# Optimization experiments

Hardware: AMD Instinct MI355X
Metric: run time of the kernel (lower is better)

Reference implementation:

```python
import jax, jax.numpy as jnp
import numpy as np
import math

N_ITEMS = 200000
N_USERS = 100000
D = 128
E_II = 3200000
E_UI = 1600000


def spmm(src, dst, val, x, n_rows):
    # out[i] = sum_{e: dst[e]==i} val[e] * x[src[e]]
    return jax.ops.segment_sum(val[:, None] * x[src], dst, num_segments=n_rows)


def leaky_relu(x):
    return jnp.where(x >= 0, x, 0.2 * x)


def setup_inputs() -> dict:
    key = jax.random.key(0)
    ks = jax.random.split(key, 16)
    d = {}
    d["b"] = 2
    d["items_emb"] = jax.random.normal(ks[0], (N_ITEMS, D), dtype=jnp.float32) * 0.1
    for i, rel in enumerate(["p2p_in", "p2p_out", "e2p_in"]):
        d[f"src_{rel}"] = jax.random.randint(ks[1 + 3 * i], (E_II,), 0, N_ITEMS, dtype=jnp.int32)
        d[f"dst_{rel}"] = jax.random.randint(ks[2 + 3 * i], (E_II,), 0, N_ITEMS, dtype=jnp.int32)
        d[f"val_{rel}"] = jax.random.uniform(ks[3 + 3 * i], (E_II,), dtype=jnp.float32) / 16.0
    d["src_ui"] = jax.random.randint(ks[10], (E_UI,), 0, N_ITEMS, dtype=jnp.int32)
    d["dst_ui"] = jax.random.randint(ks[11], (E_UI,), 0, N_USERS, dtype=jnp.int32)
    d["val_ui"] = jax.random.uniform(ks[12], (E_UI,), dtype=jnp.float32) / 16.0
    s = 1.0 / math.sqrt(D)
    d["I_p2p_in"] = jax.random.normal(ks[13], (D, D), dtype=jnp.float32) * s
    d["I_p2p_out"] = jax.random.normal(ks[14], (D, D), dtype=jnp.float32) * s
    d["I_e2p_in"] = jax.random.normal(ks[15], (D, D), dtype=jnp.float32) * s
    return d


def reference(b, items_emb, src_p2p_in, dst_p2p_in, val_p2p_in,
              src_p2p_out, dst_p2p_out, val_p2p_out,
              src_e2p_in, dst_e2p_in, val_e2p_in,
              src_ui, dst_ui, val_ui,
              I_p2p_in, I_p2p_out, I_e2p_in):
    assert b == 2  # static branch, matches torch `if b == 2`
    x = items_emb
    n = x.shape[0]
    inv_sqrt_d = 1.0 / math.sqrt(x.shape[1])

    # multi-relation sparse aggregation (torch.spmm)
    nb_in = spmm(src_p2p_in, dst_p2p_in, val_p2p_in, x, n)
    nb_out = spmm(src_p2p_out, dst_p2p_out, val_p2p_out, x, n)
    nb_e2p = spmm(src_e2p_in, dst_e2p_in, val_e2p_in, x, n)

    # gated attention over relations
    h_in = leaky_relu((x * nb_in) @ I_p2p_in)
    h_out = leaky_relu((x * nb_out) @ I_p2p_out)
    h_e2p = leaky_relu((x * nb_e2p) @ I_e2p_in)
    s_in = jnp.sum(h_in, axis=1) * inv_sqrt_d
    s_out = jnp.sum(h_out, axis=1) * inv_sqrt_d
    s_e2p = jnp.sum(h_e2p, axis=1) * inv_sqrt_d
    score = jax.nn.softmax(jnp.stack((s_in, s_out, s_e2p), axis=1), axis=1)  # [n,3]
    neighbor = (nb_in * score[:, 0:1]
                + nb_out * score[:, 1:2]
                + nb_e2p * score[:, 2:3])

    # uiGNN: user embeddings from item embeddings
    u_emb = spmm(src_ui, dst_ui, val_ui, x, N_USERS)
    return (u_emb, neighbor)
```

## Files before the change

kernel.cpp:

```cpp
#include <hip/hip_runtime.h>

#define D 128
#define N_ITEMS 200000
#define N_USERS 100000
#define TI 64

#define INV_SQRT_D 0.088388347648318447f

__global__ __launch_bounds__(256) void hist_kernel(
    const int* __restrict__ dst, unsigned* __restrict__ counts, int E)
{
    int e = blockIdx.x * 256 + threadIdx.x;
    if (e < E) atomicAdd(&counts[dst[e]], 1u);
}

__global__ __launch_bounds__(256) void scan1_kernel(
    const unsigned* __restrict__ counts, unsigned* __restrict__ offsets,
    unsigned* __restrict__ blocksums, int n)
{
    __shared__ unsigned s[256];
    int tid = threadIdx.x;
    int i = blockIdx.x * 256 + tid;
    unsigned v = (i < n) ? counts[i] : 0u;
    s[tid] = v; __syncthreads();
    #pragma unroll
    for (int off = 1; off < 256; off <<= 1) {
        unsigned t = (tid >= off) ? s[tid - off] : 0u;
        __syncthreads();
        s[tid] += t;
        __syncthreads();
    }
    if (i < n) offsets[i] = s[tid] - v;
    if (tid == 255) blocksums[blockIdx.x] = s[255];
}

__global__ __launch_bounds__(1024) void scan2_kernel(
    unsigned* __restrict__ blocksums, int nb)
{
    __shared__ unsigned s[1024];
    int tid = threadIdx.x;
    unsigned v = (tid < nb) ? blocksums[tid] : 0u;
    s[tid] = v; __syncthreads();
    #pragma unroll
    for (int off = 1; off < 1024; off <<= 1) {
        unsigned t = (tid >= off) ? s[tid - off] : 0u;
        __syncthreads();
        s[tid] += t;
        __syncthreads();
    }
    if (tid < nb) blocksums[tid] = s[tid] - v;
}

__global__ __launch_bounds__(256) void scan3_kernel(
    unsigned* __restrict__ offsets, unsigned* __restrict__ cursor,
    const unsigned* __restrict__ blocksums, int n, unsigned Etot)
{
    int i = blockIdx.x * 256 + threadIdx.x;
    if (i < n) {
        unsigned o = offsets[i] + blocksums[blockIdx.x];
        offsets[i] = o;
        cursor[i] = o;
    }
    if (i == 0) offsets[n] = Etot;
}

__global__ __launch_bounds__(256) void scatter_kernel(
    const int* __restrict__ src, const int* __restrict__ dst,
    const float* __restrict__ val, unsigned* __restrict__ cursor,
    int2* __restrict__ pairs, int E)
{
    int e = blockIdx.x * 256 + threadIdx.x;
    if (e >= E) return;
    unsigned pos = atomicAdd(&cursor[dst[e]], 1u);
    pairs[pos] = make_int2(src[e], __float_as_int(val[e]));
}

__global__ __launch_bounds__(256) void gather_spmm_kernel(
    const unsigned* __restrict__ offsets, const int2* __restrict__ pairs,
    const float4* __restrict__ x4, float4* __restrict__ out4, int nrows)
{
    int row = blockIdx.x * 8 + (threadIdx.x >> 5);
    if (row >= nrows) return;
    int lane = threadIdx.x & 31;
    unsigned j = offsets[row], end = offsets[row + 1];
    float4 acc = make_float4(0.f, 0.f, 0.f, 0.f);
    for (; j + 2 <= end; j += 2) {
        int2 p0 = pairs[j];
        int2 p1 = pairs[j + 1];
        float4 a = x4[(size_t)p0.x * 32 + lane];
        float4 b = x4[(size_t)p1.x * 32 + lane];
        float v0 = __int_as_float(p0.y), v1 = __int_as_float(p1.y);
        acc.x = fmaf(v0, a.x, acc.x); acc.y = fmaf(v0, a.y, acc.y);
        acc.z = fmaf(v0, a.z, acc.z); acc.w = fmaf(v0, a.w, acc.w);
        acc.x = fmaf(v1, b.x, acc.x); acc.y = fmaf(v1, b.y, acc.y);
        acc.z = fmaf(v1, b.z, acc.z); acc.w = fmaf(v1, b.w, acc.w);
    }
    if (j < end) {
        int2 p0 = pairs[j];
        float4 a = x4[(size_t)p0.x * 32 + lane];
        float v0 = __int_as_float(p0.y);
        acc.x = fmaf(v0, a.x, acc.x); acc.y = fmaf(v0, a.y, acc.y);
        acc.z = fmaf(v0, a.z, acc.z); acc.w = fmaf(v0, a.w, acc.w);
    }
    out4[(size_t)row * 32 + lane] = acc;
}

__global__ __launch_bounds__(256, 4) void score_combine_kernel(
    const float4* __restrict__ x4,
    float4* __restrict__ nb0,
    const float4* __restrict__ nb1, const float4* __restrict__ nb2,
    const float* __restrict__ I0, const float* __restrict__ I1,
    const float* __restrict__ I2)
{
    __shared__ float Tt[D * 65];
    __shared__ float Sred[3 * 4 * 64];
    __shared__ float Wl[TI * 3];

    const int tid  = threadIdx.x;
    const int lane = tid & 63;
    const int wv   = __builtin_amdgcn_readfirstlane(tid >> 6);
    const int ilo  = tid >> 5;
    const int dd4  = tid & 31;
    const int itemBase = blockIdx.x * TI;

    float4 xr[8];
    #pragma unroll
    for (int it = 0; it < 8; ++it) {
        int il = it * 8 + ilo;
        xr[it] = x4[(size_t)(itemBase + il) * 32 + dd4];
    }

    const float4* nbs[3] = {(const float4*)nb0, nb1, nb2};
    const float*  Is[3]  = {I0, I1, I2};

    for (int rel = 0; rel < 3; ++rel) {
        __syncthreads();
        const float4* nbp = nbs[rel];
        #pragma unroll
        for (int it = 0; it < 8; ++it) {
            int il = it * 8 + ilo;
            float4 b = nbp[(size_t)(itemBase + il) * 32 + dd4];
            float4 a = xr[it];
            int base = (dd4 * 4) * 65 + il;
            Tt[base]       = a.x * b.x;
            Tt[base + 65]  = a.y * b.y;
            Tt[base + 130] = a.z * b.z;
            Tt[base + 195] = a.w * b.w;
        }
        __syncthreads();

        const float4* Iw4 = (const float4*)Is[rel] + wv * 8;
        float4 acc[8];
        #pragma unroll
        for (int c = 0; c < 8; ++c) acc[c] = make_float4(0.f, 0.f, 0.f, 0.f);

        #pragma unroll 2
        for (int k = 0; k < D; ++k) {
            float tv = Tt[k * 65 + lane];
            #pragma unroll
            for (int c = 0; c < 8; ++c) {
                float4 iv = Iw4[k * 32 + c];
                acc[c].x = fmaf(tv, iv.x, acc[c].x);
                acc[c].y = fmaf(tv, iv.y, acc[c].y);
                acc[c].z = fmaf(tv, iv.z, acc[c].z);
                acc[c].w = fmaf(tv, iv.w, acc[c].w);
            }
        }

        float s = 0.f;
        #pragma unroll
        for (int c = 0; c < 8; ++c) {
            s += fmaxf(acc[c].x, 0.2f * acc[c].x);
            s += fmaxf(acc[c].y, 0.2f * acc[c].y);
            s += fmaxf(acc[c].z, 0.2f * acc[c].z);
            s += fmaxf(acc[c].w, 0.2f * acc[c].w);
        }
        Sred[rel * 256 + wv * 64 + lane] = s;
    }
    __syncthreads();

    if (tid < TI) {
        float sr[3];
        #pragma unroll
        for (int r = 0; r < 3; ++r)
            sr[r] = (Sred[r * 256 + tid] + Sred[r * 256 + 64 + tid] +
                     Sred[r * 256 + 128 + tid] + Sred[r * 256 + 192 + tid])
                    * INV_SQRT_D;
        float m = fmaxf(sr[0], fmaxf(sr[1], sr[2]));
        float e0 = expf(sr[0] - m), e1 = expf(sr[1] - m), e2 = expf(sr[2] - m);
        float inv = 1.f / (e0 + e1 + e2);
        Wl[tid * 3 + 0] = e0 * inv;
        Wl[tid * 3 + 1] = e1 * inv;
        Wl[tid * 3 + 2] = e2 * inv;
    }
    __syncthreads();

    #pragma unroll
    for (int it = 0; it < 8; ++it) {
        int il = it * 8 + ilo;
        size_t g = (size_t)(itemBase + il) * 32 + dd4;
        float w0 = Wl[il * 3 + 0], w1 = Wl[il * 3 + 1], w2 = Wl[il * 3 + 2];
        float4 a = nb0[g], b = nb1[g], c = nb2[g];
        float4 r;
        r.x = fmaf(w0, a.x, fmaf(w1, b.x, w2 * c.x));
        r.y = fmaf(w0, a.y, fmaf(w1, b.y, w2 * c.y));
        r.z = fmaf(w0, a.z, fmaf(w1, b.z, w2 * c.z));
        r.w = fmaf(w0, a.w, fmaf(w1, b.w, w2 * c.w));
        nb0[g] = r;
    }
}

extern "C" void kernel_launch(void* const* d_in, const int* in_sizes, int n_in,
                              void* d_out, int out_size, void* d_ws, size_t ws_size,
                              hipStream_t stream) {
    const float* x       = (const float*)d_in[1];
    const int*   src0    = (const int*)d_in[2];
    const int*   dst0    = (const int*)d_in[3];
    const float* val0    = (const float*)d_in[4];
    const int*   src1    = (const int*)d_in[5];
    const int*   dst1    = (const int*)d_in[6];
    const float* val1    = (const float*)d_in[7];
    const int*   src2    = (const int*)d_in[8];
    const int*   dst2    = (const int*)d_in[9];
    const float* val2    = (const float*)d_in[10];
    const int*   src_ui  = (const int*)d_in[11];
    const int*   dst_ui  = (const int*)d_in[12];
    const float* val_ui  = (const float*)d_in[13];
    const float* I0      = (const float*)d_in[14];
    const float* I1      = (const float*)d_in[15];
    const float* I2      = (const float*)d_in[16];

    const int E_ii = in_sizes[2];
    const int E_ui = in_sizes[11];

    float* u_emb = (float*)d_out;
    float* nb0   = (float*)d_out + (size_t)N_USERS * D;

    float*    nb1       = (float*)d_ws;
    float*    nb2       = nb1 + (size_t)N_ITEMS * D;
    unsigned* cc        = (unsigned*)(nb2 + (size_t)N_ITEMS * D);
    unsigned* offsets   = cc + N_ITEMS;
    unsigned* blocksums = offsets + N_ITEMS + 1;
    uintptr_t pu        = ((uintptr_t)(blocksums + 1024) + 15) & ~(uintptr_t)15;
    int2*     pairs_ui  = (int2*)pu;
    int2*     pairs_ii  = (int2*)d_out;

    auto build_and_gather = [&](const int* src, const int* dst, const float* val,
                                int E, int nrows, int2* pairs, float* out) {
        hipMemsetAsync(cc, 0, (size_t)nrows * sizeof(unsigned), stream);
        int gE = (E + 255) / 256;
        int gN = (nrows + 255) / 256;
        hist_kernel<<<gE, 256, 0, stream>>>(dst, cc, E);
        scan1_kernel<<<gN, 256, 0, stream>>>(cc, offsets, blocksums, nrows);
        scan2_kernel<<<1, 1024, 0, stream>>>(blocksums, gN);
        scan3_kernel<<<gN, 256, 0, stream>>>(offsets, cc, blocksums, nrows, (unsigned)E);
        scatter_kernel<<<gE, 256, 0, stream>>>(src, dst, val, cc, pairs, E);
        gather_spmm_kernel<<<(nrows + 7) / 8, 256, 0, stream>>>(
            offsets, pairs, (const float4*)x, (float4*)out, nrows);
    };

    build_and_gather(src0, dst0, val0, E_ii, N_ITEMS, pairs_ii, nb0);
    build_and_gather(src1, dst1, val1, E_ii, N_ITEMS, pairs_ii, nb1);
    build_and_gather(src2, dst2, val2, E_ii, N_ITEMS, pairs_ii, nb2);

    score_combine_kernel<<<N_ITEMS / TI, 256, 0, stream>>>(
        (const float4*)x, (float4*)nb0, (const float4*)nb1, (const float4*)nb2,
        I0, I1, I2);

    build_and_gather(src_ui, dst_ui, val_ui, E_ui, N_USERS, pairs_ui, u_emb);
}
```

Before: 2.558 ms.

## Batch CSR histogram and scan across all relations, unroll gather, swizzle LDS

All four relations (three item-item and one user-item) now share one padded count array. A single histogram kernel, one memset and one three-kernel scan build CSR offsets for every relation, replacing four separate build pipelines. The histogram and scatter kernels handle two edges per thread, and the gather SpMM loop is unrolled to four edges with a higher occupancy hint. The score kernel's transposed LDS tile uses an XOR swizzle to reduce bank conflicts. In exchange, the code relies on padded per-relation offsets and reuses nb2 as the pairs buffer for the user relation, which is safe only because nb2 is consumed before that scatter runs.

```diff
diff --git a/kernel.cpp b/kernel.cpp
--- a/kernel.cpp
+++ b/kernel.cpp
@@ -5,23 +5,48 @@
 #define N_USERS 100000
 #define TI 64
 
+#define PADN 200192
+#define PADU 100096
+#define NT   (3 * PADN + PADU)
+#define NBLK (NT / 256)
+#define RSB0 0
+#define RSB1 (PADN / 256)
+#define RSB2 (2 * PADN / 256)
+#define RSB3 (3 * PADN / 256)
+
 #define INV_SQRT_D 0.088388347648318447f
 
-__global__ __launch_bounds__(256) void hist_kernel(
-    const int* __restrict__ dst, unsigned* __restrict__ counts, int E)
-{
-    int e = blockIdx.x * 256 + threadIdx.x;
-    if (e < E) atomicAdd(&counts[dst[e]], 1u);
+__global__ __launch_bounds__(256) void hist_all_kernel(
+    const int* __restrict__ d0, const int* __restrict__ d1,
+    const int* __restrict__ d2, const int* __restrict__ du,
+    unsigned* __restrict__ counts, int Eii, int Eui, int gh)
+{
+    int bi = blockIdx.x;
+    const int* dp; int E; int base; int b0;
+    if (bi < 3 * gh) {
+        int r = bi / gh;
+        dp = (r == 0) ? d0 : (r == 1 ? d1 : d2);
+        E = Eii; base = r * PADN; b0 = r * gh;
+    } else {
+        dp = du; E = Eui; base = 3 * PADN; b0 = 3 * gh;
+    }
+    int e = ((bi - b0) * 256 + threadIdx.x) * 2;
+    if (e + 2 <= E) {
+        int a = dp[e], b = dp[e + 1];
+        atomicAdd(&counts[base + a], 1u);
+        atomicAdd(&counts[base + b], 1u);
+    } else if (e < E) {
+        atomicAdd(&counts[base + dp[e]], 1u);
+    }
 }
 
 __global__ __launch_bounds__(256) void scan1_kernel(
-    const unsigned* __restrict__ counts, unsigned* __restrict__ offsets,
-    unsigned* __restrict__ blocksums, int n)
+    unsigned* __restrict__ data, unsigned* __restrict__ blocksums)
 {
     __shared__ unsigned s[256];
     int tid = threadIdx.x;
     int i = blockIdx.x * 256 + tid;
-    unsigned v = (i < n) ? counts[i] : 0u;
+    unsigned v = data[i];
     s[tid] = v; __syncthreads();
     #pragma unroll
     for (int off = 1; off < 256; off <<= 1) {
@@ -30,17 +55,23 @@
         s[tid] += t;
         __syncthreads();
     }
-    if (i < n) offsets[i] = s[tid] - v;
+    data[i] = s[tid] - v;
     if (tid == 255) blocksums[blockIdx.x] = s[255];
 }
 
 __global__ __launch_bounds__(1024) void scan2_kernel(
-    unsigned* __restrict__ blocksums, int nb)
+    unsigned* __restrict__ bs, int nb)
 {
     __shared__ unsigned s[1024];
     int tid = threadIdx.x;
-    unsigned v = (tid < nb) ? blocksums[tid] : 0u;
-    s[tid] = v; __syncthreads();
+    int base = tid * 4;
+    unsigned v[4]; unsigned tot = 0;
+    #pragma unroll
+    for (int t = 0; t < 4; ++t) {
+        v[t] = (base + t < nb) ? bs[base + t] : 0u;
+        tot += v[t];
+    }
+    s[tid] = tot; __syncthreads();
     #pragma unroll
     for (int off = 1; off < 1024; off <<= 1) {
         unsigned t = (tid >= off) ? s[tid - off] : 0u;
@@ -48,20 +79,25 @@
         s[tid] += t;
         __syncthreads();
     }
-    if (tid < nb) blocksums[tid] = s[tid] - v;
+    unsigned run = s[tid] - tot;
+    #pragma unroll
+    for (int t = 0; t < 4; ++t) {
+        unsigned old = v[t];
+        if (base + t < nb) bs[base + t] = run;
+        run += old;
+    }
 }
 
 __global__ __launch_bounds__(256) void scan3_kernel(
-    unsigned* __restrict__ offsets, unsigned* __restrict__ cursor,
-    const unsigned* __restrict__ blocksums, int n, unsigned Etot)
+    unsigned* __restrict__ offs, unsigned* __restrict__ cursor,
+    const unsigned* __restrict__ bs)
 {
     int i = blockIdx.x * 256 + threadIdx.x;
-    if (i < n) {
-        unsigned o = offsets[i] + blocksums[blockIdx.x];
-        offsets[i] = o;
-        cursor[i] = o;
-    }
-    if (i == 0) offsets[n] = Etot;
+    int rel = (i < 3 * PADN) ? (i / PADN) : 3;
+    int rsb = (rel == 0) ? RSB0 : (rel == 1 ? RSB1 : (rel == 2 ? RSB2 : RSB3));
+    unsigned o = offs[i] + bs[blockIdx.x] - bs[rsb];
+    offs[i] = o;
+    cursor[i] = o;
 }
 
 __global__ __launch_bounds__(256) void scatter_kernel(
@@ -69,13 +105,22 @@
     const float* __restrict__ val, unsigned* __restrict__ cursor,
     int2* __restrict__ pairs, int E)
 {
-    int e = blockIdx.x * 256 + threadIdx.x;
-    if (e >= E) return;
-    unsigned pos = atomicAdd(&cursor[dst[e]], 1u);
-    pairs[pos] = make_int2(src[e], __float_as_int(val[e]));
-}
-
-__global__ __launch_bounds__(256) void gather_spmm_kernel(
+    int e = (blockIdx.x * 256 + threadIdx.x) * 2;
+    if (e + 2 <= E) {
+        int s0 = src[e], s1 = src[e + 1];
+        int d0 = dst[e], d1 = dst[e + 1];
+        float v0 = val[e], v1 = val[e + 1];
+        unsigned p0 = atomicAdd(&cursor[d0], 1u);
+        unsigned p1 = atomicAdd(&cursor[d1], 1u);
+        pairs[p0] = make_int2(s0, __float_as_int(v0));
+        pairs[p1] = make_int2(s1, __float_as_int(v1));
+    } else if (e < E) {
+        unsigned p = atomicAdd(&cursor[dst[e]], 1u);
+        pairs[p] = make_int2(src[e], __float_as_int(val[e]));
+    }
+}
+
+__global__ __launch_bounds__(256, 8) void gather_spmm_kernel(
     const unsigned* __restrict__ offsets, const int2* __restrict__ pairs,
     const float4* __restrict__ x4, float4* __restrict__ out4, int nrows)
 {
@@ -84,7 +129,27 @@
     int lane = threadIdx.x & 31;
     unsigned j = offsets[row], end = offsets[row + 1];
     float4 acc = make_float4(0.f, 0.f, 0.f, 0.f);
-    for (; j + 2 <= end; j += 2) {
+    for (; j + 4 <= end; j += 4) {
+        int2 p0 = pairs[j];
+        int2 p1 = pairs[j + 1];
+        int2 p2 = pairs[j + 2];
+        int2 p3 = pairs[j + 3];
+        float4 a = x4[(size_t)p0.x * 32 + lane];
+        float4 b = x4[(size_t)p1.x * 32 + lane];
+        float4 c = x4[(size_t)p2.x * 32 + lane];
+        float4 d = x4[(size_t)p3.x * 32 + lane];
+        float v0 = __int_as_float(p0.y), v1 = __int_as_float(p1.y);
+        float v2 = __int_as_float(p2.y), v3 = __int_as_float(p3.y);
+        acc.x = fmaf(v0, a.x, acc.x); acc.y = fmaf(v0, a.y, acc.y);
+        acc.z = fmaf(v0, a.z, acc.z); acc.w = fmaf(v0, a.w, acc.w);
+        acc.x = fmaf(v1, b.x, acc.x); acc.y = fmaf(v1, b.y, acc.y);
+        acc.z = fmaf(v1, b.z, acc.z); acc.w = fmaf(v1, b.w, acc.w);
+        acc.x = fmaf(v2, c.x, acc.x); acc.y = fmaf(v2, c.y, acc.y);
+        acc.z = fmaf(v2, c.z, acc.z); acc.w = fmaf(v2, c.w, acc.w);
+        acc.x = fmaf(v3, d.x, acc.x); acc.y = fmaf(v3, d.y, acc.y);
+        acc.z = fmaf(v3, d.z, acc.z); acc.w = fmaf(v3, d.w, acc.w);
+    }
+    if (j + 2 <= end) {
         int2 p0 = pairs[j];
         int2 p1 = pairs[j + 1];
         float4 a = x4[(size_t)p0.x * 32 + lane];
@@ -94,6 +159,7 @@
         acc.z = fmaf(v0, a.z, acc.z); acc.w = fmaf(v0, a.w, acc.w);
         acc.x = fmaf(v1, b.x, acc.x); acc.y = fmaf(v1, b.y, acc.y);
         acc.z = fmaf(v1, b.z, acc.z); acc.w = fmaf(v1, b.w, acc.w);
+        j += 2;
     }
     if (j < end) {
         int2 p0 = pairs[j];
@@ -122,6 +188,7 @@
     const int ilo  = tid >> 5;
     const int dd4  = tid & 31;
     const int itemBase = blockIdx.x * TI;
+    const int sswz = (dd4 >> 3) & 3;
 
     float4 xr[8];
     #pragma unroll
@@ -141,7 +208,8 @@
             int il = it * 8 + ilo;
             float4 b = nbp[(size_t)(itemBase + il) * 32 + dd4];
             float4 a = xr[it];
-            int base = (dd4 * 4) * 65 + il;
+            int ilx = il ^ (sswz << 1);
+            int base = (dd4 * 4) * 65 + ilx;
             Tt[base]       = a.x * b.x;
             Tt[base + 65]  = a.y * b.y;
             Tt[base + 130] = a.z * b.z;
@@ -156,7 +224,7 @@
 
         #pragma unroll 2
         for (int k = 0; k < D; ++k) {
-            float tv = Tt[k * 65 + lane];
+            float tv = Tt[k * 65 + (lane ^ (((k >> 5) & 3) << 1))];
             #pragma unroll
             for (int c = 0; c < 8; ++c) {
                 float4 iv = Iw4[k * 32 + c];
@@ -238,34 +306,42 @@
 
     float*    nb1       = (float*)d_ws;
     float*    nb2       = nb1 + (size_t)N_ITEMS * D;
-    unsigned* cc        = (unsigned*)(nb2 + (size_t)N_ITEMS * D);
-    unsigned* offsets   = cc + N_ITEMS;
-    unsigned* blocksums = offsets + N_ITEMS + 1;
-    uintptr_t pu        = ((uintptr_t)(blocksums + 1024) + 15) & ~(uintptr_t)15;
-    int2*     pairs_ui  = (int2*)pu;
+    unsigned* counts    = (unsigned*)(nb2 + (size_t)N_ITEMS * D);
+    unsigned* cursor    = counts + NT;
+    unsigned* blocksums = cursor + NT;
     int2*     pairs_ii  = (int2*)d_out;
-
-    auto build_and_gather = [&](const int* src, const int* dst, const float* val,
-                                int E, int nrows, int2* pairs, float* out) {
-        hipMemsetAsync(cc, 0, (size_t)nrows * sizeof(unsigned), stream);
-        int gE = (E + 255) / 256;
-        int gN = (nrows + 255) / 256;
-        hist_kernel<<<gE, 256, 0, stream>>>(dst, cc, E);
-        scan1_kernel<<<gN, 256, 0, stream>>>(cc, offsets, blocksums, nrows);
-        scan2_kernel<<<1, 1024, 0, stream>>>(blocksums, gN);
-        scan3_kernel<<<gN, 256, 0, stream>>>(offsets, cc, blocksums, nrows, (unsigned)E);
-        scatter_kernel<<<gE, 256, 0, stream>>>(src, dst, val, cc, pairs, E);
-        gather_spmm_kernel<<<(nrows + 7) / 8, 256, 0, stream>>>(
-            offsets, pairs, (const float4*)x, (float4*)out, nrows);
-    };
-
-    build_and_gather(src0, dst0, val0, E_ii, N_ITEMS, pairs_ii, nb0);
-    build_and_gather(src1, dst1, val1, E_ii, N_ITEMS, pairs_ii, nb1);
-    build_and_gather(src2, dst2, val2, E_ii, N_ITEMS, pairs_ii, nb2);
+    int2*     pairs_ui  = (int2*)nb2;
+
+    const int gh  = (E_ii + 511) / 512;
+    const int ghu = (E_ui + 511) / 512;
+    const int gsE  = (E_ii + 511) / 512;
+    const int gsEu = (E_ui + 511) / 512;
+
+    hipMemsetAsync(counts, 0, (size_t)NT * sizeof(unsigned), stream);
+    hist_all_kernel<<<3 * gh + ghu, 256, 0, stream>>>(
+        dst0, dst1, dst2, dst_ui, counts, E_ii, E_ui, gh);
+    scan1_kernel<<<NBLK, 256, 0, stream>>>(counts, blocksums);
+    scan2_kernel<<<1, 1024, 0, stream>>>(blocksums, NBLK);
+    scan3_kernel<<<NBLK, 256, 0, stream>>>(counts, cursor, blocksums);
+
+    const int* srcs[3] = {src0, src1, src2};
+    const int* dsts[3] = {dst0, dst1, dst2};
+    const float* vals[3] = {val0, val1, val2};
+    float* outs[3] = {nb0, nb1, nb2};
+    for (int r = 0; r < 3; ++r) {
+        scatter_kernel<<<gsE, 256, 0, stream>>>(
+            srcs[r], dsts[r], vals[r], cursor + r * PADN, pairs_ii, E_ii);
+        gather_spmm_kernel<<<(N_ITEMS + 7) / 8, 256, 0, stream>>>(
+            counts + r * PADN, pairs_ii, (const float4*)x, (float4*)outs[r],
+            N_ITEMS);
+    }
 
     score_combine_kernel<<<N_ITEMS / TI, 256, 0, stream>>>(
         (const float4*)x, (float4*)nb0, (const float4*)nb1, (const float4*)nb2,
         I0, I1, I2);
 
-    build_and_gather(src_ui, dst_ui, val_ui, E_ui, N_USERS, pairs_ui, u_emb);
-}
+    scatter_kernel<<<gsEu, 256, 0, stream>>>(
+        src_ui, dst_ui, val_ui, cursor + 3 * PADN, pairs_ui, E_ui);
+    gather_spmm_kernel<<<(N_USERS + 7) / 8, 256, 0, stream>>>(
+        counts + 3 * PADN, pairs_ui, (const float4*)x, (float4*)u_emb, N_USERS);
+}
```

Measured after the change: 2.618 ms. 2.3% more time.
